# Kernel optimization log

Hardware: AMD Instinct MI355X
Metric: run time of the kernel (lower is better)

## Reference

```python
import jax, jax.numpy as jnp
import numpy as np

N = 50000
E = 800000
IN_C = 128
HID = 32
HEADS = 4
G = 512      # number of graphs in batch
OUT_C = 100
NEG_SLOPE = 0.2
EPS = 1e-16


def _gat_params(key, f_in, heads, c):
    k1, k2, k3, k4 = jax.random.split(key, 4)
    s = 1.0 / np.sqrt(f_in)
    return {
        'W': jax.random.uniform(k1, (heads * c, f_in), jnp.float32, -s, s),
        'att_src': jax.random.normal(k2, (heads, c), jnp.float32) * 0.1,
        'att_dst': jax.random.normal(k3, (heads, c), jnp.float32) * 0.1,
        'b': jnp.zeros((heads * c,), jnp.float32),
    }


def setup_inputs() -> dict:
    key = jax.random.key(0)
    ks = jax.random.split(key, 8)
    x = jax.random.normal(ks[0], (N, IN_C), jnp.float32)
    edge_index = jax.random.randint(ks[1], (2, E), 0, N, jnp.int64)
    batch = jnp.sort(jax.random.randint(ks[2], (N,), 0, G, jnp.int64))
    p1 = _gat_params(ks[3], IN_C, HEADS, HID)
    p2 = _gat_params(ks[4], HEADS * HID, HEADS, HID)
    p3 = _gat_params(ks[5], HEADS * HID, HEADS, HID)
    s = 1.0 / np.sqrt(HEADS * HID)
    fc_W = jax.random.uniform(ks[6], (OUT_C, HEADS * HID), jnp.float32, -s, s)
    fc_b = jnp.zeros((OUT_C,), jnp.float32)
    return {
        'x': x, 'edge_index': edge_index, 'batch': batch,
        'W1': p1['W'], 'as1': p1['att_src'], 'ad1': p1['att_dst'], 'b1': p1['b'],
        'W2': p2['W'], 'as2': p2['att_src'], 'ad2': p2['att_dst'], 'b2': p2['b'],
        'W3': p3['W'], 'as3': p3['att_src'], 'ad3': p3['att_dst'], 'b3': p3['b'],
        'fc_W': fc_W, 'fc_b': fc_b,
    }


def gat_conv(x, src, dst, W, att_src, att_dst, b):
    # x: [N, F_in] -> h: [N, H, C]
    h = (x @ W.T).reshape(N, HEADS, HID)
    a_src = jnp.einsum('nhc,hc->nh', h, att_src)   # [N, H]
    a_dst = jnp.einsum('nhc,hc->nh', h, att_dst)
    alpha = a_src[src] + a_dst[dst]                 # [E', H]
    alpha = jax.nn.leaky_relu(alpha, NEG_SLOPE)
    # segment softmax over incoming edges of each dst node
    m = jax.ops.segment_max(alpha, dst, num_segments=N)
    alpha = jnp.exp(alpha - m[dst])
    denom = jax.ops.segment_sum(alpha, dst, num_segments=N)
    alpha = alpha / (denom[dst] + EPS)
    msg = alpha[:, :, None] * h[src]                # [E', H, C]
    out = jax.ops.segment_sum(msg, dst, num_segments=N)
    return out.reshape(N, HEADS * HID) + b


def reference(x, edge_index, batch,
              W1, as1, ad1, b1, W2, as2, ad2, b2, W3, as3, ad3, b3,
              fc_W, fc_b):
    # add self loops (PyG GATConv default)
    loops = jnp.arange(N, dtype=edge_index.dtype)
    src = jnp.concatenate([edge_index[0], loops])
    dst = jnp.concatenate([edge_index[1], loops])
    h = jax.nn.elu(gat_conv(x, src, dst, W1, as1, ad1, b1))
    h = jax.nn.elu(gat_conv(h, src, dst, W2, as2, ad2, b2))
    h = jax.nn.elu(gat_conv(h, src, dst, W3, as3, ad3, b3))
    # global mean pool over graphs
    sums = jax.ops.segment_sum(h, batch, num_segments=G)        # [G, H*C]
    cnts = jax.ops.segment_sum(jnp.ones((N,), h.dtype), batch, num_segments=G)
    pooled = sums / jnp.maximum(cnts, 1.0)[:, None]
    # dropout p=0.5 is identity in eval mode
    return pooled @ fc_W.T + fc_b
```

## Files before the change

### kernel.cpp

```cpp
#include <hip/hip_runtime.h>
#include <math.h>

#define NN 50000
#define EE 800000
#define GG 512
#define OUTC 100
#define NEG 0.2f
#define STRIDE 64
#define NPART 8
#define PRNG (NN / NPART)
#define PCHUNK 4096
#define SCAT_BLOCKS (NPART * 196)

typedef __attribute__((ext_vector_type(8))) short bf16x8;
typedef __attribute__((ext_vector_type(8))) short s16x8;
typedef __attribute__((ext_vector_type(8))) unsigned short us8;
typedef __attribute__((ext_vector_type(4))) float f32x4;

__device__ inline ushort f2bf(float v) {
  unsigned u = __float_as_uint(v);
  unsigned r = (u + 0x7fff + ((u >> 16) & 1)) >> 16;
  return (ushort)r;
}

__global__ __launch_bounds__(256) void k_scatter_prep(const int* __restrict__ ei,
    int* __restrict__ cursor, ushort* __restrict__ srcs,
    const float* __restrict__ W0, const float* __restrict__ W1, const float* __restrict__ W2,
    const float* __restrict__ as0, const float* __restrict__ as1, const float* __restrict__ as2,
    const float* __restrict__ ad0, const float* __restrict__ ad1, const float* __restrict__ ad2,
    ushort* __restrict__ hi, ushort* __restrict__ lo) {
  if (blockIdx.x < SCAT_BLOCKS) {
    int part = blockIdx.x & (NPART - 1);
    int chunk = blockIdx.x >> 3;
    int plo = part * PRNG, phi = plo + PRNG;
    int base = chunk * PCHUNK;
    for (int i = threadIdx.x; i < PCHUNK; i += 256) {
      int e = base + i;
      if (e >= EE) break;
      int d = ei[EE + e];
      if (d < plo || d >= phi) continue;
      int s = ei[e];
      int pos = atomicAdd(&cursor[d], 1);
      if (pos < STRIDE) srcs[(d << 6) + pos] = (ushort)s;
    }
  } else {
    int pb = blockIdx.x - SCAT_BLOCKS;
    int layer = pb / 68, bx = pb % 68;
    const float* W  = (layer == 0) ? W0 : (layer == 1) ? W1 : W2;
    const float* av = (layer == 0) ? as0 : (layer == 1) ? as1 : as2;
    const float* dv = (layer == 0) ? ad0 : (layer == 1) ? ad1 : ad2;
    ushort* hiL = hi + (size_t)layer * 144 * 128;
    ushort* loL = lo + (size_t)layer * 144 * 128;
    int idx = bx * 256 + threadIdx.x;
    if (bx < 64) {
      float v = W[idx];
      ushort hb = f2bf(v);
      float hf = __uint_as_float(((unsigned)hb) << 16);
      hiL[idx] = hb;
      loL[idx] = f2bf(v - hf);
    } else {
      int j2 = idx - 64 * 256;
      int j = j2 >> 7, k = j2 & 127;
      int head = j & 3;
      const float* vec = (j < 4) ? &av[head * 32] : &dv[head * 32];
      float dot = 0.f;
#pragma unroll
      for (int c = 0; c < 32; c++) dot += W[(head * 32 + c) * 128 + k] * vec[c];
      ushort hb = f2bf(dot);
      float hf = __uint_as_float(((unsigned)hb) << 16);
      hiL[(128 + j) * 128 + k] = hb;
      loL[(128 + j) * 128 + k] = f2bf(dot - hf);
      hiL[(136 + j) * 128 + k] = 0;
      loL[(136 + j) * 128 + k] = 0;
    }
  }
}

__global__ __launch_bounds__(256) void k_gemm_mfma(const float* __restrict__ feat,
    const ushort* __restrict__ Whi, const ushort* __restrict__ Wlo,
    short* __restrict__ hq, float* __restrict__ scalef,
    float* __restrict__ asrcf, float* __restrict__ adstf) {
  int t = threadIdx.x;
  int wave = t >> 6, lane = t & 63;
  int quad = lane >> 4, r16 = lane & 15;
  int n0 = blockIdx.x * 128;

  float4 a[2][8];
#pragma unroll
  for (int mt = 0; mt < 2; mt++) {
    int row = n0 + wave * 32 + mt * 16 + r16;
    int lrow = min(row, NN - 1);
    const float4* fp = (const float4*)&feat[(size_t)lrow * 128 + quad * 8];
#pragma unroll
    for (int ks = 0; ks < 4; ks++) {
      a[mt][2 * ks]     = fp[ks * 8];
      a[mt][2 * ks + 1] = fp[ks * 8 + 1];
    }
  }

  f32x4 acc[2][9];
#pragma unroll
  for (int mt = 0; mt < 2; mt++)
#pragma unroll
    for (int nt = 0; nt < 9; nt++) acc[mt][nt] = (f32x4)0.f;

#pragma unroll
  for (int ks = 0; ks < 4; ks++) {
    bf16x8 ah[2], al[2];
#pragma unroll
    for (int mt = 0; mt < 2; mt++) {
      float4 va = a[mt][2 * ks], vb = a[mt][2 * ks + 1];
      float vv[8] = {va.x, va.y, va.z, va.w, vb.x, vb.y, vb.z, vb.w};
      us8 hh, ll;
#pragma unroll
      for (int j = 0; j < 8; j++) {
        ushort hb = f2bf(vv[j]);
        float hf = __uint_as_float(((unsigned)hb) << 16);
        hh[j] = hb;
        ll[j] = (ushort)(__float_as_uint(vv[j] - hf) >> 16);
      }
      ah[mt] = (bf16x8)hh;
      al[mt] = (bf16x8)ll;
    }
#pragma unroll
    for (int nt = 0; nt < 9; nt++) {
      int wrow = (nt < 8) ? (nt * 16 + r16) : (128 + r16);
      size_t wo = (size_t)wrow * 128 + ks * 32 + quad * 8;
      bf16x8 bh = *(const bf16x8*)&Whi[wo];
      bf16x8 bl = *(const bf16x8*)&Wlo[wo];
#pragma unroll
      for (int mt = 0; mt < 2; mt++) {
        acc[mt][nt] = __builtin_amdgcn_mfma_f32_16x16x32_bf16(ah[mt], bh, acc[mt][nt], 0, 0, 0);
        acc[mt][nt] = __builtin_amdgcn_mfma_f32_16x16x32_bf16(al[mt], bh, acc[mt][nt], 0, 0, 0);
        acc[mt][nt] = __builtin_amdgcn_mfma_f32_16x16x32_bf16(ah[mt], bl, acc[mt][nt], 0, 0, 0);
      }
    }
  }

#pragma unroll
  for (int mt = 0; mt < 2; mt++) {
#pragma unroll
    for (int reg = 0; reg < 4; reg++) {
      float am = 0.f;
#pragma unroll
      for (int nt = 0; nt < 8; nt++) am = fmaxf(am, fabsf(acc[mt][nt][reg]));
#pragma unroll
      for (int off = 1; off < 16; off <<= 1) am = fmaxf(am, __shfl_xor(am, off));
      int node = n0 + wave * 32 + mt * 16 + quad * 4 + reg;
      if (node < NN) {
        float amc = fmaxf(am, 1e-20f);
        float rq = 32767.f / amc;
        if (r16 == 0) scalef[node] = amc * (1.f / 32767.f);
        if (r16 < 4) asrcf[node * 4 + r16] = acc[mt][8][reg];
        else if (r16 < 8) adstf[node * 4 + r16 - 4] = acc[mt][8][reg];
        short* dq = &hq[(size_t)node * 128 + r16];
#pragma unroll
        for (int nt = 0; nt < 8; nt++)
          dq[nt * 16] = (short)__float2int_rn(acc[mt][nt][reg] * rq);
      }
    }
  }
}

__global__ __launch_bounds__(256) void k_gather(const short* __restrict__ hq,
    const float* __restrict__ scalef,
    const float4* __restrict__ asrc, const float4* __restrict__ adst,
    const int* __restrict__ cursor, const ushort* __restrict__ srcs,
    const float* __restrict__ bias, float* __restrict__ outf) {
  __shared__ int s_src[4][4][16];
  __shared__ float s_w[4][4][72];
  __shared__ float s_e[4][4][72];

  int wave = threadIdx.x >> 6, lane = threadIdx.x & 63;
  int grp = lane >> 4;
  int gl = lane & 15;
  int node = blockIdx.x * 16 + wave * 4 + grp;

  int deg = 0, e0 = 0;
  float4 ad = make_float4(0.f, 0.f, 0.f, 0.f);
  if (node < NN) {
    deg = min(cursor[node], STRIDE);
    e0 = node << 6;
    ad = adst[node];
  }
  int c0 = gl << 3;
  int head = gl >> 2;

  float acc[8];
#pragma unroll
  for (int i = 0; i < 8; i++) acc[i] = 0.f;
  float wsum = 0.f;

  if (node < NN) {
    float4 a = asrc[node];
    float sc = scalef[node];
    float v, w0, w1, w2, w3;
    v = a.x + ad.x; v = v > 0.f ? v : NEG * v; w0 = expf(v);
    v = a.y + ad.y; v = v > 0.f ? v : NEG * v; w1 = expf(v);
    v = a.z + ad.z; v = v > 0.f ? v : NEG * v; w2 = expf(v);
    v = a.w + ad.w; v = v > 0.f ? v : NEG * v; w3 = expf(v);
    float wh = (head == 0) ? w0 : (head == 1) ? w1 : (head == 2) ? w2 : w3;
    wsum = wh;
    float ws = wh * sc;
    s16x8 qs = *(const s16x8*)&hq[(node << 7) + c0];
#pragma unroll
    for (int i = 0; i < 8; i++) acc[i] = ws * (float)qs[i];
  }

  int rounds = (deg + 15) >> 4;
  for (int r = 0; r < rounds; r++) {
    int base = r << 4;
    int j = base + gl;
    int sn = 0;
    float w0 = 0.f, w1 = 0.f, w2 = 0.f, w3 = 0.f, sc = 0.f;
    if (j < deg) {
      sn = srcs[e0 + j];
      float4 a = asrc[sn];
      sc = scalef[sn];
      float v;
      v = a.x + ad.x; v = v > 0.f ? v : NEG * v; w0 = expf(v);
      v = a.y + ad.y; v = v > 0.f ? v : NEG * v; w1 = expf(v);
      v = a.z + ad.z; v = v > 0.f ? v : NEG * v; w2 = expf(v);
      v = a.w + ad.w; v = v > 0.f ? v : NEG * v; w3 = expf(v);
    }
    s_src[wave][grp][gl] = sn << 7;
    float* wp = &s_w[wave][grp][gl << 2];
    wp[0] = w0 * sc; wp[1] = w1 * sc; wp[2] = w2 * sc; wp[3] = w3 * sc;
    float* ep = &s_e[wave][grp][gl << 2];
    ep[0] = w0; ep[1] = w1; ep[2] = w2; ep[3] = w3;

    int cnt = min(16, deg - base);
    int cntp = (cnt + 3) & ~3;
    for (int k = 0; k < cntp; k += 4) {
      int ra = s_src[wave][grp][k + 0];
      int rb = s_src[wave][grp][k + 1];
      int rc = s_src[wave][grp][k + 2];
      int rd = s_src[wave][grp][k + 3];
      float wa = s_w[wave][grp][((k + 0) << 2) | head];
      float wb = s_w[wave][grp][((k + 1) << 2) | head];
      float wc = s_w[wave][grp][((k + 2) << 2) | head];
      float wd = s_w[wave][grp][((k + 3) << 2) | head];
      wsum += s_e[wave][grp][((k + 0) << 2) | head]
            + s_e[wave][grp][((k + 1) << 2) | head]
            + s_e[wave][grp][((k + 2) << 2) | head]
            + s_e[wave][grp][((k + 3) << 2) | head];
      s16x8 qa = *(const s16x8*)&hq[ra + c0];
      s16x8 qb = *(const s16x8*)&hq[rb + c0];
      s16x8 qc = *(const s16x8*)&hq[rc + c0];
      s16x8 qd = *(const s16x8*)&hq[rd + c0];
#pragma unroll
      for (int i = 0; i < 8; i++) acc[i] = fmaf(wa, (float)qa[i], acc[i]);
#pragma unroll
      for (int i = 0; i < 8; i++) acc[i] = fmaf(wb, (float)qb[i], acc[i]);
#pragma unroll
      for (int i = 0; i < 8; i++) acc[i] = fmaf(wc, (float)qc[i], acc[i]);
#pragma unroll
      for (int i = 0; i < 8; i++) acc[i] = fmaf(wd, (float)qd[i], acc[i]);
    }
  }

  if (node < NN) {
    float rcp = 1.f / (wsum + 1e-16f);
    float o[8];
#pragma unroll
    for (int i = 0; i < 8; i++) {
      float v = acc[i] * rcp + bias[c0 + i];
      o[i] = v > 0.f ? v : expm1f(v);
    }
    *(float4*)&outf[(size_t)node * 128 + c0] = make_float4(o[0], o[1], o[2], o[3]);
    *(float4*)&outf[(size_t)node * 128 + c0 + 4] = make_float4(o[4], o[5], o[6], o[7]);
  }
}

__global__ __launch_bounds__(128) void k_pool(const float* __restrict__ feat,
    const int* __restrict__ batch, float* __restrict__ pooled, float* __restrict__ cnt) {
  int n0 = blockIdx.x * 32;
  int c = threadIdx.x;
  float acc = 0.f; int curg = -1;
  for (int i = 0; i < 32; i++) {
    int n = n0 + i;
    if (n >= NN) break;
    int g = batch[n];
    if (g != curg) {
      if (curg >= 0) atomicAdd(&pooled[curg * 128 + c], acc);
      acc = 0.f; curg = g;
    }
    acc += feat[n * 128 + c];
  }
  if (curg >= 0) atomicAdd(&pooled[curg * 128 + c], acc);
  if (threadIdx.x == 0) {
    float cc = 0.f; int cg = -1;
    for (int i = 0; i < 32; i++) {
      int n = n0 + i;
      if (n >= NN) break;
      int g = batch[n];
      if (g != cg) { if (cg >= 0) atomicAdd(&cnt[cg], cc); cc = 0.f; cg = g; }
      cc += 1.f;
    }
    if (cg >= 0) atomicAdd(&cnt[cg], cc);
  }
}

__global__ __launch_bounds__(128) void k_fc(const float* __restrict__ pooled,
    const float* __restrict__ cnt, const float* __restrict__ fcW,
    const float* __restrict__ fcb, float* __restrict__ out) {
  int g = blockIdx.x;
  __shared__ float p[128];
  int t = threadIdx.x;
  float inv = 1.0f / fmaxf(cnt[g], 1.0f);
  p[t] = pooled[g * 128 + t] * inv;
  __syncthreads();
  if (t < OUTC) {
    float acc = fcb[t];
    const float4* wr = (const float4*)&fcW[t * 128];
    const float4* pp = (const float4*)p;
#pragma unroll
    for (int i = 0; i < 32; i++) {
      float4 w = wr[i], pv = pp[i];
      acc = fmaf(w.x, pv.x, fmaf(w.y, pv.y, fmaf(w.z, pv.z, fmaf(w.w, pv.w, acc))));
    }
    out[g * OUTC + t] = acc;
  }
}

extern "C" void kernel_launch(void* const* d_in, const int* in_sizes, int n_in,
                              void* d_out, int out_size, void* d_ws, size_t ws_size,
                              hipStream_t stream) {
  const float* x    = (const float*)d_in[0];
  const int*   ei   = (const int*)d_in[1];
  const int*   batch= (const int*)d_in[2];
  const float* W1   = (const float*)d_in[3];
  const float* as1  = (const float*)d_in[4];
  const float* ad1  = (const float*)d_in[5];
  const float* b1   = (const float*)d_in[6];
  const float* W2   = (const float*)d_in[7];
  const float* as2  = (const float*)d_in[8];
  const float* ad2  = (const float*)d_in[9];
  const float* b2   = (const float*)d_in[10];
  const float* W3   = (const float*)d_in[11];
  const float* as3  = (const float*)d_in[12];
  const float* ad3  = (const float*)d_in[13];
  const float* b3   = (const float*)d_in[14];
  const float* fcW  = (const float*)d_in[15];
  const float* fcb  = (const float*)d_in[16];
  float* out = (float*)d_out;

  char* p = (char*)d_ws;
  auto alloc = [&](size_t bytes) { char* r = p; p += (bytes + 255) & ~(size_t)255; return r; };
  short* hq     = (short*)alloc((size_t)NN * 128 * 2);
  float* scalef = (float*)alloc((size_t)NN * 4);
  float* buf0   = (float*)alloc((size_t)NN * 128 * 4);
  float* asrc   = (float*)alloc((size_t)NN * 4 * 4);
  float* adst   = (float*)alloc((size_t)NN * 4 * 4);
  char*  zbase  = p;
  int*   cursor = (int*)alloc((size_t)NN * 4);
  float* pooled = (float*)alloc((size_t)GG * 128 * 4);
  float* cnt    = (float*)alloc((size_t)GG * 4);
  size_t zlen   = (size_t)(p - zbase);
  ushort* srcs  = (ushort*)alloc((size_t)NN * STRIDE * 2);
  ushort* whi   = (ushort*)alloc((size_t)3 * 144 * 128 * 2);
  ushort* wlo   = (ushort*)alloc((size_t)3 * 144 * 128 * 2);

  hipMemsetAsync(zbase, 0, zlen, stream);

  k_scatter_prep<<<SCAT_BLOCKS + 204, 256, 0, stream>>>(ei, cursor, srcs,
      W1, W2, W3, as1, as2, as3, ad1, ad2, ad3, whi, wlo);

  const float* bs[3] = {b1, b2, b3};
  const float* fin = x;
  for (int l = 0; l < 3; l++) {
    k_gemm_mfma<<<(NN + 127) / 128, 256, 0, stream>>>(fin,
        whi + (size_t)l * 144 * 128, wlo + (size_t)l * 144 * 128,
        hq, scalef, asrc, adst);
    k_gather<<<(NN + 15) / 16, 256, 0, stream>>>(hq, scalef,
        (const float4*)asrc, (const float4*)adst,
        cursor, srcs, bs[l], buf0);
    fin = buf0;
  }
  k_pool<<<(NN + 31) / 32, 128, 0, stream>>>(buf0, batch, pooled, cnt);
  k_fc<<<GG, 128, 0, stream>>>(pooled, cnt, fcW, fcb, out);
}
```

Baseline: 364.9 us.

## Emit bf16 hi/lo split from gather and fuse mean-pool into last gather

The gather kernel now writes its activations already split into bf16 hi/lo halves, so the next GEMM loads them directly instead of loading fp32 and splitting in registers. The last layer's gather does the pooling itself with per-node atomic adds into the graph sums and counts, which removes the separate pool kernel and one full fp32 write and read of the activations. The cost is many more atomics to the pooled buffer, one per element of every node instead of run-length reduced, which could contend because the nodes of a graph are contiguous.

```diff
diff --git a/kernel.cpp b/kernel.cpp
--- a/kernel.cpp
+++ b/kernel.cpp
@@ -76,7 +76,9 @@
   }
 }
 
-__global__ __launch_bounds__(256) void k_gemm_mfma(const float* __restrict__ feat,
+template <bool SPLIT>
+__global__ __launch_bounds__(256) void k_gemm_mfma(const float* __restrict__ featf,
+    const ushort* __restrict__ fhi, const ushort* __restrict__ flo,
     const ushort* __restrict__ Whi, const ushort* __restrict__ Wlo,
     short* __restrict__ hq, float* __restrict__ scalef,
     float* __restrict__ asrcf, float* __restrict__ adstf) {
@@ -85,16 +87,36 @@
   int quad = lane >> 4, r16 = lane & 15;
   int n0 = blockIdx.x * 128;
 
-  float4 a[2][8];
+  bf16x8 ahh[2][4], all[2][4];
 #pragma unroll
   for (int mt = 0; mt < 2; mt++) {
     int row = n0 + wave * 32 + mt * 16 + r16;
     int lrow = min(row, NN - 1);
-    const float4* fp = (const float4*)&feat[(size_t)lrow * 128 + quad * 8];
-#pragma unroll
-    for (int ks = 0; ks < 4; ks++) {
-      a[mt][2 * ks]     = fp[ks * 8];
-      a[mt][2 * ks + 1] = fp[ks * 8 + 1];
+    if (SPLIT) {
+      const us8* hp = (const us8*)&fhi[(size_t)lrow * 128];
+      const us8* lp = (const us8*)&flo[(size_t)lrow * 128];
+#pragma unroll
+      for (int ks = 0; ks < 4; ks++) {
+        ahh[mt][ks] = (bf16x8)hp[ks * 4 + quad];
+        all[mt][ks] = (bf16x8)lp[ks * 4 + quad];
+      }
+    } else {
+      const float4* fp = (const float4*)&featf[(size_t)lrow * 128 + quad * 8];
+#pragma unroll
+      for (int ks = 0; ks < 4; ks++) {
+        float4 va = fp[ks * 8], vb = fp[ks * 8 + 1];
+        float vv[8] = {va.x, va.y, va.z, va.w, vb.x, vb.y, vb.z, vb.w};
+        us8 hh, ll;
+#pragma unroll
+        for (int j = 0; j < 8; j++) {
+          ushort hb = f2bf(vv[j]);
+          float hf = __uint_as_float(((unsigned)hb) << 16);
+          hh[j] = hb;
+          ll[j] = (ushort)(__float_as_uint(vv[j] - hf) >> 16);
+        }
+        ahh[mt][ks] = (bf16x8)hh;
+        all[mt][ks] = (bf16x8)ll;
+      }
     }
   }
 
@@ -106,22 +128,6 @@
 
 #pragma unroll
   for (int ks = 0; ks < 4; ks++) {
-    bf16x8 ah[2], al[2];
-#pragma unroll
-    for (int mt = 0; mt < 2; mt++) {
-      float4 va = a[mt][2 * ks], vb = a[mt][2 * ks + 1];
-      float vv[8] = {va.x, va.y, va.z, va.w, vb.x, vb.y, vb.z, vb.w};
-      us8 hh, ll;
-#pragma unroll
-      for (int j = 0; j < 8; j++) {
-        ushort hb = f2bf(vv[j]);
-        float hf = __uint_as_float(((unsigned)hb) << 16);
-        hh[j] = hb;
-        ll[j] = (ushort)(__float_as_uint(vv[j] - hf) >> 16);
-      }
-      ah[mt] = (bf16x8)hh;
-      al[mt] = (bf16x8)ll;
-    }
 #pragma unroll
     for (int nt = 0; nt < 9; nt++) {
       int wrow = (nt < 8) ? (nt * 16 + r16) : (128 + r16);
@@ -130,9 +136,9 @@
       bf16x8 bl = *(const bf16x8*)&Wlo[wo];
 #pragma unroll
       for (int mt = 0; mt < 2; mt++) {
-        acc[mt][nt] = __builtin_amdgcn_mfma_f32_16x16x32_bf16(ah[mt], bh, acc[mt][nt], 0, 0, 0);
-        acc[mt][nt] = __builtin_amdgcn_mfma_f32_16x16x32_bf16(al[mt], bh, acc[mt][nt], 0, 0, 0);
-        acc[mt][nt] = __builtin_amdgcn_mfma_f32_16x16x32_bf16(ah[mt], bl, acc[mt][nt], 0, 0, 0);
+        acc[mt][nt] = __builtin_amdgcn_mfma_f32_16x16x32_bf16(ahh[mt][ks], bh, acc[mt][nt], 0, 0, 0);
+        acc[mt][nt] = __builtin_amdgcn_mfma_f32_16x16x32_bf16(all[mt][ks], bh, acc[mt][nt], 0, 0, 0);
+        acc[mt][nt] = __builtin_amdgcn_mfma_f32_16x16x32_bf16(ahh[mt][ks], bl, acc[mt][nt], 0, 0, 0);
       }
     }
   }
@@ -162,11 +168,13 @@
   }
 }
 
-__global__ __launch_bounds__(256) void k_gather(const short* __restrict__ hq,
+template <bool POOL>
+__global__ __launch_bounds__(256) void k_gather_t(const short* __restrict__ hq,
     const float* __restrict__ scalef,
     const float4* __restrict__ asrc, const float4* __restrict__ adst,
     const int* __restrict__ cursor, const ushort* __restrict__ srcs,
-    const float* __restrict__ bias, float* __restrict__ outf) {
+    const float* __restrict__ bias, ushort* __restrict__ fhi, ushort* __restrict__ flo,
+    const int* __restrict__ batch, float* __restrict__ pooled, float* __restrict__ cntg) {
   __shared__ int s_src[4][4][16];
   __shared__ float s_w[4][4][72];
   __shared__ float s_e[4][4][72];
@@ -267,37 +275,24 @@
       float v = acc[i] * rcp + bias[c0 + i];
       o[i] = v > 0.f ? v : expm1f(v);
     }
-    *(float4*)&outf[(size_t)node * 128 + c0] = make_float4(o[0], o[1], o[2], o[3]);
-    *(float4*)&outf[(size_t)node * 128 + c0 + 4] = make_float4(o[4], o[5], o[6], o[7]);
-  }
-}
-
-__global__ __launch_bounds__(128) void k_pool(const float* __restrict__ feat,
-    const int* __restrict__ batch, float* __restrict__ pooled, float* __restrict__ cnt) {
-  int n0 = blockIdx.x * 32;
-  int c = threadIdx.x;
-  float acc = 0.f; int curg = -1;
-  for (int i = 0; i < 32; i++) {
-    int n = n0 + i;
-    if (n >= NN) break;
-    int g = batch[n];
-    if (g != curg) {
-      if (curg >= 0) atomicAdd(&pooled[curg * 128 + c], acc);
-      acc = 0.f; curg = g;
-    }
-    acc += feat[n * 128 + c];
-  }
-  if (curg >= 0) atomicAdd(&pooled[curg * 128 + c], acc);
-  if (threadIdx.x == 0) {
-    float cc = 0.f; int cg = -1;
-    for (int i = 0; i < 32; i++) {
-      int n = n0 + i;
-      if (n >= NN) break;
-      int g = batch[n];
-      if (g != cg) { if (cg >= 0) atomicAdd(&cnt[cg], cc); cc = 0.f; cg = g; }
-      cc += 1.f;
-    }
-    if (cg >= 0) atomicAdd(&cnt[cg], cc);
+    if (POOL) {
+      int g = batch[node];
+      float* pr = &pooled[(size_t)g * 128 + c0];
+#pragma unroll
+      for (int i = 0; i < 8; i++) atomicAdd(&pr[i], o[i]);
+      if (gl == 0) atomicAdd(&cntg[g], 1.f);
+    } else {
+      us8 hh, ll;
+#pragma unroll
+      for (int i = 0; i < 8; i++) {
+        ushort hb = f2bf(o[i]);
+        float hf = __uint_as_float(((unsigned)hb) << 16);
+        hh[i] = hb;
+        ll[i] = (ushort)(__float_as_uint(o[i] - hf) >> 16);
+      }
+      *(us8*)&fhi[(size_t)node * 128 + c0] = hh;
+      *(us8*)&flo[(size_t)node * 128 + c0] = ll;
+    }
   }
 }
 
@@ -349,13 +344,14 @@
   auto alloc = [&](size_t bytes) { char* r = p; p += (bytes + 255) & ~(size_t)255; return r; };
   short* hq     = (short*)alloc((size_t)NN * 128 * 2);
   float* scalef = (float*)alloc((size_t)NN * 4);
-  float* buf0   = (float*)alloc((size_t)NN * 128 * 4);
+  ushort* fhi   = (ushort*)alloc((size_t)NN * 128 * 2);
+  ushort* flo   = (ushort*)alloc((size_t)NN * 128 * 2);
   float* asrc   = (float*)alloc((size_t)NN * 4 * 4);
   float* adst   = (float*)alloc((size_t)NN * 4 * 4);
   char*  zbase  = p;
   int*   cursor = (int*)alloc((size_t)NN * 4);
   float* pooled = (float*)alloc((size_t)GG * 128 * 4);
-  float* cnt    = (float*)alloc((size_t)GG * 4);
+  float* cntg   = (float*)alloc((size_t)GG * 4);
   size_t zlen   = (size_t)(p - zbase);
   ushort* srcs  = (ushort*)alloc((size_t)NN * STRIDE * 2);
   ushort* whi   = (ushort*)alloc((size_t)3 * 144 * 128 * 2);
@@ -366,17 +362,26 @@
   k_scatter_prep<<<SCAT_BLOCKS + 204, 256, 0, stream>>>(ei, cursor, srcs,
       W1, W2, W3, as1, as2, as3, ad1, ad2, ad3, whi, wlo);
 
-  const float* bs[3] = {b1, b2, b3};
-  const float* fin = x;
-  for (int l = 0; l < 3; l++) {
-    k_gemm_mfma<<<(NN + 127) / 128, 256, 0, stream>>>(fin,
-        whi + (size_t)l * 144 * 128, wlo + (size_t)l * 144 * 128,
-        hq, scalef, asrc, adst);
-    k_gather<<<(NN + 15) / 16, 256, 0, stream>>>(hq, scalef,
-        (const float4*)asrc, (const float4*)adst,
-        cursor, srcs, bs[l], buf0);
-    fin = buf0;
-  }
-  k_pool<<<(NN + 31) / 32, 128, 0, stream>>>(buf0, batch, pooled, cnt);
-  k_fc<<<GG, 128, 0, stream>>>(pooled, cnt, fcW, fcb, out);
-}
+  int gemm_grid = (NN + 127) / 128;
+  int gath_grid = (NN + 15) / 16;
+
+  k_gemm_mfma<false><<<gemm_grid, 256, 0, stream>>>(x, nullptr, nullptr,
+      whi, wlo, hq, scalef, asrc, adst);
+  k_gather_t<false><<<gath_grid, 256, 0, stream>>>(hq, scalef,
+      (const float4*)asrc, (const float4*)adst, cursor, srcs, b1,
+      fhi, flo, batch, pooled, cntg);
+
+  k_gemm_mfma<true><<<gemm_grid, 256, 0, stream>>>(nullptr, fhi, flo,
+      whi + (size_t)144 * 128, wlo + (size_t)144 * 128, hq, scalef, asrc, adst);
+  k_gather_t<false><<<gath_grid, 256, 0, stream>>>(hq, scalef,
+      (const float4*)asrc, (const float4*)adst, cursor, srcs, b2,
+      fhi, flo, batch, pooled, cntg);
+
+  k_gemm_mfma<true><<<gemm_grid, 256, 0, stream>>>(nullptr, fhi, flo,
+      whi + (size_t)2 * 144 * 128, wlo + (size_t)2 * 144 * 128, hq, scalef, asrc, adst);
+  k_gather_t<true><<<gath_grid, 256, 0, stream>>>(hq, scalef,
+      (const float4*)asrc, (const float4*)adst, cursor, srcs, b3,
+      nullptr, nullptr, batch, pooled, cntg);
+
+  k_fc<<<GG, 128, 0, stream>>>(pooled, cntg, fcW, fcb, out);
+}
```

Result: slower. 600.9 us (+64.7%).
